# Kernel tuning notes

Hardware: AMD Instinct MI355X
Metric: run time of the kernel (lower is better)

The kernel has to match this reference:

```python
import jax, jax.numpy as jnp
import numpy as np
from jax import lax

NEG = -1e30  # effectively log(0), safe in float32 over long accumulations


def setup_inputs() -> dict:
    key = jax.random.key(0)
    k1, k2, k3, k4, k5 = jax.random.split(key, 5)
    T, B, L, S = 2048, 64, 64, 256
    inputs = jax.random.normal(k1, (T, B, L), dtype=jnp.float32)
    # module initializes transition to zeros; use small random values for a
    # non-degenerate reference (zeros make transition terms vanish)
    transition = 0.01 * jax.random.normal(k2, (L, L), dtype=jnp.float32)
    targets = jax.random.randint(k3, (B, S), 0, L)
    input_lengths = jax.random.randint(k4, (B,), T // 2, T + 1)
    target_lengths = jax.random.randint(k5, (B,), S // 4, S + 1)
    return {"inputs": inputs, "transition": transition, "targets": targets,
            "input_lengths": input_lengths, "target_lengths": target_lengths}


def _fcc(inputs, trans, input_lengths):
    # Fully-connected (partition) score: logsumexp over all label paths.
    # trans[i, j] = score of transitioning from label j to label i.
    T, B, L = inputs.shape
    def step(alpha, xt):
        x, t = xt
        # new[b,i] = x[b,i] + logsumexp_j(alpha[b,j] + trans[i,j])
        new = x + jax.scipy.special.logsumexp(alpha[:, None, :] + trans[None, :, :], axis=-1)
        alpha = jnp.where((t < input_lengths)[:, None], new, alpha)
        return alpha, None
    alpha, _ = lax.scan(step, inputs[0], (inputs[1:], jnp.arange(1, T)))
    return jax.scipy.special.logsumexp(alpha, axis=-1)  # [B]


def _fac(inputs, trans, targets, input_lengths, target_lengths):
    # Force-aligned score: logsumexp over monotonic alignments of targets.
    T, B, L = inputs.shape
    S = targets.shape[1]
    emit = inputs[:, jnp.arange(B)[:, None], targets]          # [T,B,S]
    self_tr = trans[targets, targets]                           # [B,S] stay score
    prev = jnp.concatenate([targets[:, :1], targets[:, :-1]], axis=1)
    move_tr = trans[targets, prev].at[:, 0].set(NEG)            # [B,S] advance score
    alpha0 = jnp.full((B, S), NEG, jnp.float32).at[:, 0].set(emit[0, :, 0])
    def step(alpha, et):
        e, t = et
        shifted = jnp.concatenate([jnp.full((B, 1), NEG, jnp.float32), alpha[:, :-1]], axis=1)
        new = e + jnp.logaddexp(alpha + self_tr, shifted + move_tr)
        alpha = jnp.where((t < input_lengths)[:, None], new, alpha)
        return alpha, None
    alpha, _ = lax.scan(step, alpha0, (emit[1:], jnp.arange(1, T)))
    return alpha[jnp.arange(B), target_lengths - 1]             # [B]


def reference(inputs, transition, targets, input_lengths, target_lengths):
    full = _fcc(inputs, transition, input_lengths)
    aligned = _fac(inputs, transition, targets, input_lengths, target_lengths)
    return jnp.mean(full - aligned)  # reduction='mean'
```

## Files before the change

kernel.cpp:

```cpp
#include <hip/hip_runtime.h>
#include <math.h>


constexpr int T_ = 2048, B_ = 64, L_ = 64, S_ = 256;
constexpr int CSEG = 64, NSEG = 32;
constexpr int FCH = 16;
constexpr float LN2 = 0.6931471805599453f;

typedef __bf16 bf16x8 __attribute__((ext_vector_type(8)));
typedef __bf16 bf16x4 __attribute__((ext_vector_type(4)));
typedef float f32x16 __attribute__((ext_vector_type(16)));

constexpr size_t OFF_SCALE = (size_t)NSEG * B_ * 4096 * 2;
constexpr size_t OFF_FULL = OFF_SCALE + (size_t)NSEG * B_ * 4;
constexpr size_t OFF_FWD = OFF_FULL + B_ * 4;
constexpr size_t OFF_BWD = OFF_FWD + (size_t)B_ * 256 * 8;
constexpr size_t OFF_LF = OFF_BWD + (size_t)B_ * 256 * 8;
constexpr size_t OFF_LB = OFF_LF + B_ * 4;

__device__ __forceinline__ float wave_max64(float v) {
#pragma unroll
  for (int off = 1; off < 64; off <<= 1) v = fmaxf(v, __shfl_xor(v, off, 64));
  return v;
}
__device__ __forceinline__ float wave_sum64(float v) {
#pragma unroll
  for (int off = 1; off < 64; off <<= 1) v += __shfl_xor(v, off, 64);
  return v;
}
__device__ __forceinline__ double wave_max64d(double v) {
#pragma unroll
  for (int off = 1; off < 64; off <<= 1) v = fmax(v, __shfl_xor(v, off, 64));
  return v;
}

struct P1shm {
  __align__(16) float xs[CSEG][64];
  __align__(16) float m_arr[CSEG];
  __align__(16) float redmax[4];
  __align__(16) __bf16 P[2][64 * 68];
};
struct FACshm {
  __align__(16) float E[2][FCH][64];
  __align__(16) float Eg[2][FCH][256];
  __align__(16) float m_fac[2][FCH];
  __align__(16) float mg[2][FCH];
};
union KU {
  P1shm p1;
  FACshm fac;
};

__global__ __launch_bounds__(256) void asg_k1(
    const float* __restrict__ inputs, const float* __restrict__ trans,
    const int* __restrict__ targets, const int* __restrict__ ilen,
    const int* __restrict__ tlenp, char* __restrict__ ws) {
  __shared__ KU u;
  const int tid = threadIdx.x, lane = tid & 63, wv = tid >> 6;
  const int bid = blockIdx.x;
  float* scales = (float*)(ws + OFF_SCALE);

  if (bid < 2 * B_) {
    const bool isfwd = (bid < B_);
    const int b = bid & 63;
    const int len = ilen[b];
    const int tl = tlenp[b];
    const int TS = (len - 1) >> 1;
    double* vecout = (double*)(ws + (isfwd ? OFF_FWD : OFF_BWD)) + b * 256;
    float* Lout = (float*)(ws + (isfwd ? OFF_LF : OFF_LB));

    int tg0 = 0, tg1 = 0, tg2 = 0, tg3 = 0;
    if (wv == 0 || wv == 2) {
      int4 t4 = *(const int4*)(targets + b * S_ + lane * 4);
      tg0 = t4.x; tg1 = t4.y; tg2 = t4.z; tg3 = t4.w;
    }
    auto stage = [&](int c, int buf) {
#pragma unroll
      for (int i = 0; i < 4; ++i) {
        int f = lane + 64 * i;
        int r = f >> 4, c4 = f & 15;
        int t = c * FCH + r;
        if (t > T_ - 1) t = T_ - 1;
        float4 v = *(const float4*)(inputs + (size_t)t * (B_ * L_) + b * L_ +
                                    c4 * 4);
        float m = fmaxf(fmaxf(v.x, v.y), fmaxf(v.z, v.w));
#pragma unroll
        for (int off = 1; off < 16; off <<= 1)
          m = fmaxf(m, __shfl_xor(m, off, 64));
        v.x = __expf(v.x - m); v.y = __expf(v.y - m);
        v.z = __expf(v.z - m); v.w = __expf(v.w - m);
        *(float4*)&u.fac.E[buf][r][c4 * 4] = v;
        if ((lane & 15) == 0) u.fac.m_fac[buf][r] = m;
      }
    };
    auto regather = [&](int c, int buf) {
#pragma unroll 4
      for (int r = 0; r < FCH; ++r) {
        float4 h;
        h.x = u.fac.E[buf][r][tg0]; h.y = u.fac.E[buf][r][tg1];
        h.z = u.fac.E[buf][r][tg2]; h.w = u.fac.E[buf][r][tg3];
        *(float4*)&u.fac.Eg[buf][r][lane * 4] = h;
      }
      if (lane < FCH) u.fac.mg[buf][lane] = u.fac.m_fac[buf][lane];
    };

    if (isfwd) {
      double sw0 = 0, sw1 = 0, sw2 = 0, sw3 = 0;
      double mw0 = 0, mw1 = 0, mw2 = 0, mw3 = 0;
      if (wv == 0) {
        int tgm1 = (lane > 0) ? targets[b * S_ + lane * 4 - 1] : 0;
        sw0 = exp((double)trans[tg0 * 64 + tg0]);
        sw1 = exp((double)trans[tg1 * 64 + tg1]);
        sw2 = exp((double)trans[tg2 * 64 + tg2]);
        sw3 = exp((double)trans[tg3 * 64 + tg3]);
        mw0 = (lane == 0) ? 0.0 : exp((double)trans[tg0 * 64 + tgm1]);
        mw1 = exp((double)trans[tg1 * 64 + tg0]);
        mw2 = exp((double)trans[tg2 * 64 + tg1]);
        mw3 = exp((double)trans[tg3 * 64 + tg2]);
      }
      if (wv == 1) { stage(0, 0); stage(1, 1); }
      __syncthreads();
      if (wv == 2) regather(0, 0);
      __syncthreads();

      double d0 = 0.0, d1 = 0.0, d2 = 0.0, d3 = 0.0, shv = 0.0;
      float Lacc = 0.0f;
      const int addr_up = ((lane + 63) & 63) << 2;
      if (wv == 0) {
        if (lane == 0) d0 = (double)u.fac.Eg[0][0][0];
        Lacc = u.fac.mg[0][0];
        __builtin_amdgcn_s_setprio(1);
      }
      for (int c = 0; 16 * c <= TS; ++c) {
        const int buf = c & 1;
        if (wv == 1) {
          if (16 * (c + 2) <= TS) stage(c + 2, buf);
        } else if (wv == 2) {
          if (16 * (c + 1) <= TS) regather(c + 1, buf ^ 1);
        } else if (wv == 0) {
          if (c) {
            double dmax = wave_max64d(fmax(fmax(d0, d1), fmax(d2, d3)));
            long long lm = __double_as_longlong(dmax);
            int ex = (int)((lm >> 52) & 0x7FF);
            double M = __longlong_as_double((long long)(2046 - ex) << 52);
            d0 *= M; d1 *= M; d2 *= M; d3 *= M; shv *= M;
            Lacc += (float)(ex - 1023) * LN2;
          }
          const int r0 = (c == 0) ? 1 : 0;
          const int rmax = min(FCH, TS + 1 - 16 * c);
          float4 eH = *(const float4*)&u.fac.Eg[buf][r0][lane * 4];
          float mH = u.fac.mg[buf][r0];
          const int r1 = min(r0 + 1, FCH - 1);
          float4 pH = *(const float4*)&u.fac.Eg[buf][r1][lane * 4];
          float pM = u.fac.mg[buf][r1];
          for (int r = r0; r < rmax; ++r) {
            const int rn = min(r + 2, FCH - 1);
            float4 nH = *(const float4*)&u.fac.Eg[buf][rn][lane * 4];
            float nM = u.fac.mg[buf][rn];
            double nd3 = (double)eH.w * fma(mw3, d2, sw3 * d3);
            long long l3 = __double_as_longlong(nd3);
            int slo = __builtin_amdgcn_ds_bpermute(addr_up, (int)l3);
            int shi = __builtin_amdgcn_ds_bpermute(addr_up, (int)(l3 >> 32));
            double nd0 = (double)eH.x * fma(mw0, shv, sw0 * d0);
            double nd1 = (double)eH.y * fma(mw1, d0, sw1 * d1);
            double nd2 = (double)eH.z * fma(mw2, d1, sw2 * d2);
            d0 = nd0; d1 = nd1; d2 = nd2; d3 = nd3;
            shv = __longlong_as_double(((long long)shi << 32) |
                                       (unsigned int)slo);
            Lacc += mH;
            eH = pH; mH = pM; pH = nH; pM = nM;
          }
        }
        __syncthreads();
      }
      if (wv == 0) {
        __builtin_amdgcn_s_setprio(0);
        vecout[lane * 4 + 0] = d0; vecout[lane * 4 + 1] = d1;
        vecout[lane * 4 + 2] = d2; vecout[lane * 4 + 3] = d3;
        if (lane == 0) Lout[b] = Lacc;
      }
    } else {
      double sw0 = 0, sw1 = 0, sw2 = 0, sw3 = 0;
      double mv0 = 0, mv1 = 0, mv2 = 0, mv3 = 0;
      if (wv == 0) {
        int tg4 = (lane < 63) ? targets[b * S_ + lane * 4 + 4] : 0;
        sw0 = exp((double)trans[tg0 * 64 + tg0]);
        sw1 = exp((double)trans[tg1 * 64 + tg1]);
        sw2 = exp((double)trans[tg2 * 64 + tg2]);
        sw3 = exp((double)trans[tg3 * 64 + tg3]);
        mv0 = exp((double)trans[tg1 * 64 + tg0]);
        mv1 = exp((double)trans[tg2 * 64 + tg1]);
        mv2 = exp((double)trans[tg3 * 64 + tg2]);
        mv3 = (lane < 63) ? exp((double)trans[tg4 * 64 + tg3]) : 0.0;
      }
      const int cmax = (len - 1) >> 4;
      const int cmin = (TS + 1) >> 4;
      if (wv == 1) {
        stage(cmax, cmax & 1);
        if (cmax - 1 >= cmin) stage(cmax - 1, (cmax - 1) & 1);
      }
      __syncthreads();
      if (wv == 2) regather(cmax, cmax & 1);
      __syncthreads();

      const int idx = tl - 1;
      double b0 = 0, b1 = 0, b2 = 0, b3 = 0, g0cur = 0, shg = 0;
      float Lacc = 0.0f;
      const int addr_dn = ((lane + 1) & 63) << 2;
      if (wv == 0) {
        b0 = (lane * 4 + 0 == idx) ? 1.0 : 0.0;
        b1 = (lane * 4 + 1 == idx) ? 1.0 : 0.0;
        b2 = (lane * 4 + 2 == idx) ? 1.0 : 0.0;
        b3 = (lane * 4 + 3 == idx) ? 1.0 : 0.0;
        const int rh0 = (len - 1) & 15;
        float e0x = u.fac.Eg[cmax & 1][rh0][lane * 4];
        g0cur = (double)e0x * b0;
        long long lg = __double_as_longlong(g0cur);
        int slo = __builtin_amdgcn_ds_bpermute(addr_dn, (int)lg);
        int shi = __builtin_amdgcn_ds_bpermute(addr_dn, (int)(lg >> 32));
        shg = __longlong_as_double(((long long)shi << 32) | (unsigned int)slo);
        __builtin_amdgcn_s_setprio(1);
      }
      for (int c = cmax; c >= cmin; --c) {
        const int buf = c & 1;
        if (wv == 1) {
          if (c - 2 >= cmin) stage(c - 2, buf);
        } else if (wv == 2) {
          if (c - 1 >= cmin) regather(c - 1, buf ^ 1);
        } else if (wv == 0) {
          if (c != cmax) {
            double dmax = wave_max64d(fmax(fmax(b0, b1), fmax(b2, b3)));
            long long lm = __double_as_longlong(dmax);
            int ex = (int)((lm >> 52) & 0x7FF);
            double M = __longlong_as_double((long long)(2046 - ex) << 52);
            b0 *= M; b1 *= M; b2 *= M; b3 *= M; g0cur *= M; shg *= M;
            Lacc += (float)(ex - 1023) * LN2;
          }
          const int rhi = (c == cmax) ? ((len - 1) & 15) : FCH - 1;
          const int rlo = max(0, (TS + 1) - 16 * c);
          float4 eH = *(const float4*)&u.fac.Eg[buf][rhi][lane * 4];
          float mH = u.fac.mg[buf][rhi];
          const int r1 = max(rhi - 1, rlo);
          float4 pH = *(const float4*)&u.fac.Eg[buf][r1][lane * 4];
          float pM = u.fac.mg[buf][r1];
          for (int r = rhi; r >= rlo; --r) {
            const int rn = max(r - 2, rlo);
            float4 nH = *(const float4*)&u.fac.Eg[buf][rn][lane * 4];
            float nM = u.fac.mg[buf][rn];
            double g1 = (double)eH.y * b1;
            double g2 = (double)eH.z * b2;
            double g3 = (double)eH.w * b3;
            double nb0 = fma(mv0, g1, sw0 * g0cur);
            double nb1 = fma(mv1, g2, sw1 * g1);
            double nb2 = fma(mv2, g3, sw2 * g2);
            double nb3 = fma(mv3, shg, sw3 * g3);
            double g0n = (double)pH.x * nb0;
            long long lg2 = __double_as_longlong(g0n);
            int slo2 = __builtin_amdgcn_ds_bpermute(addr_dn, (int)lg2);
            int shi2 = __builtin_amdgcn_ds_bpermute(addr_dn, (int)(lg2 >> 32));
            b0 = nb0; b1 = nb1; b2 = nb2; b3 = nb3;
            g0cur = g0n;
            shg = __longlong_as_double(((long long)shi2 << 32) |
                                       (unsigned int)slo2);
            Lacc += mH;
            eH = pH; mH = pM; pH = nH; pM = nM;
          }
        }
        __syncthreads();
      }
      if (wv == 0) {
        __builtin_amdgcn_s_setprio(0);
        vecout[lane * 4 + 0] = b0; vecout[lane * 4 + 1] = b1;
        vecout[lane * 4 + 2] = b2; vecout[lane * 4 + 3] = b3;
        if (lane == 0) Lout[b] = Lacc;
      }
    }
    return;
  }

  const int sid = bid - 2 * B_;
  const int b = sid >> 5, s = sid & 31;
  const int t0 = 1 + s * CSEG;
  const int len = ilen[b];
  int ke = min(CSEG, T_ - t0);
  ke = min(ke, len - t0);
  if (ke < 0) ke = 0;

#pragma unroll
  for (int i = 0; i < 4; ++i) {
    int f4 = tid + 256 * i;
    int r = f4 >> 4, c4 = f4 & 15;
    int t = t0 + r;
    if (t > T_ - 1) t = T_ - 1;
    float4 v = *(const float4*)(inputs + (size_t)t * (B_ * L_) + b * L_ + c4 * 4);
    *(float4*)(&u.p1.xs[r][c4 * 4]) = v;
  }
  __syncthreads();
#pragma unroll
  for (int rr = 0; rr < 16; ++rr) {
    int r = wv * 16 + rr;
    float v = wave_max64(u.p1.xs[r][lane]);
    if (lane == 0) u.p1.m_arr[r] = v;
  }
  __syncthreads();
#pragma unroll
  for (int i = 0; i < 4; ++i) {
    int f4 = tid + 256 * i;
    int r = f4 >> 4, c4 = f4 & 15;
    float m = u.p1.m_arr[r];
    float4 v = *(float4*)(&u.p1.xs[r][c4 * 4]);
    v.x = __expf(v.x - m); v.y = __expf(v.y - m);
    v.z = __expf(v.z - m); v.w = __expf(v.w - m);
    *(float4*)(&u.p1.xs[r][c4 * 4]) = v;
  }
  for (int i = tid; i < 64 * 68; i += 256) u.p1.P[0][i] = (__bf16)0.0f;
  __syncthreads();
  if (tid < 64) u.p1.P[0][tid * 68 + tid] = (__bf16)1.0f;

  const int ma = wv >> 1, nb = wv & 1;
  const int arow = 32 * ma + (lane & 31);
  const int hh = lane >> 5;
  const int coln = 32 * nb + (lane & 31);
  float Wf[4][8];
#pragma unroll
  for (int kc = 0; kc < 4; ++kc) {
    const float* tp = trans + arow * 64 + kc * 16 + hh * 8;
#pragma unroll
    for (int j = 0; j < 8; ++j) Wf[kc][j] = __expf(tp[j]);
  }

  float lsres = 0.0f;
  int cur = 0;
  for (int k = 0; k < ke; ++k) {
    __syncthreads();
    float scf = 1.0f;
    if ((k & 7) == 0 && k != 0) {
      float mm = fmaxf(fmaxf(u.p1.redmax[0], u.p1.redmax[1]),
                       fmaxf(u.p1.redmax[2], u.p1.redmax[3]));
      scf = __builtin_amdgcn_rcpf(mm);
      lsres += __logf(mm);
    }
    const float srow = u.p1.xs[k][arow] * scf;
    bf16x8 A[4], Bf[4];
    const __bf16* Pc = u.p1.P[cur];
#pragma unroll
    for (int kc = 0; kc < 4; ++kc) {
#pragma unroll
      for (int j = 0; j < 8; ++j) A[kc][j] = (__bf16)(Wf[kc][j] * srow);
      const __bf16* p = Pc + coln * 68 + kc * 16 + hh * 8;
      bf16x4 lo = *(const bf16x4*)p;
      bf16x4 hi = *(const bf16x4*)(p + 4);
      Bf[kc] = __builtin_shufflevector(lo, hi, 0, 1, 2, 3, 4, 5, 6, 7);
    }
    f32x16 acc;
#pragma unroll
    for (int e = 0; e < 16; ++e) acc[e] = 0.0f;
    acc = __builtin_amdgcn_mfma_f32_32x32x16_bf16(A[0], Bf[0], acc, 0, 0, 0);
    acc = __builtin_amdgcn_mfma_f32_32x32x16_bf16(A[1], Bf[1], acc, 0, 0, 0);
    acc = __builtin_amdgcn_mfma_f32_32x32x16_bf16(A[2], Bf[2], acc, 0, 0, 0);
    acc = __builtin_amdgcn_mfma_f32_32x32x16_bf16(A[3], Bf[3], acc, 0, 0, 0);
    __bf16* Pn = u.p1.P[cur ^ 1];
#pragma unroll
    for (int q = 0; q < 4; ++q) {
      const int i0 = 32 * ma + 8 * q + 4 * hh;
      bf16x4 w;
      w[0] = (__bf16)acc[4 * q + 0]; w[1] = (__bf16)acc[4 * q + 1];
      w[2] = (__bf16)acc[4 * q + 2]; w[3] = (__bf16)acc[4 * q + 3];
      *(bf16x4*)(Pn + coln * 68 + i0) = w;
    }
    if ((k & 7) == 7) {
      float mx = acc[0];
#pragma unroll
      for (int e = 1; e < 16; ++e) mx = fmaxf(mx, acc[e]);
      mx = wave_max64(mx);
      if (lane == 0) u.p1.redmax[wv] = mx;
    }
    cur ^= 1;
  }
  __syncthreads();
  __bf16* G = ((__bf16*)ws) + (size_t)sid * 4096;
  const __bf16* Pf = u.p1.P[cur];
  for (int i = tid; i < 4096; i += 256) G[i] = Pf[(i >> 6) * 68 + (i & 63)];
  if (wv == 0) {
    float mt = (lane < ke) ? u.p1.m_arr[lane] : 0.0f;
    float msum = wave_sum64(mt);
    if (lane == 0) scales[sid] = msum + lsres;
  }
}

__global__ __launch_bounds__(128) void asg_k2(const float* __restrict__ inputs,
                                              char* __restrict__ ws) {
  __shared__ __align__(16) float Gl[2][64][68];
  __shared__ __align__(16) float Eb[64];
  const int tid = threadIdx.x, lane = tid & 63, wv = tid >> 6;
  const int b = blockIdx.x;
  const __bf16* M = (const __bf16*)ws;
  const float* scales = (const float*)(ws + OFF_SCALE);
  float* full = (float*)(ws + OFF_FULL);

  auto stage = [&](int s, int buf) {
    const __bf16* g = M + ((size_t)(b * NSEG + s)) * 4096 + lane * 64;
#pragma unroll
    for (int q = 0; q < 8; ++q) {
      bf16x8 v = *(const bf16x8*)(g + q * 8);
      float4 f0{(float)v[0], (float)v[1], (float)v[2], (float)v[3]};
      float4 f1{(float)v[4], (float)v[5], (float)v[6], (float)v[7]};
      *(float4*)&Gl[buf][lane][q * 8] = f0;
      *(float4*)&Gl[buf][lane][q * 8 + 4] = f1;
    }
  };

  float Ev = 0.0f, ls = 0.0f;
  if (wv == 0) {
    float x0 = inputs[b * L_ + lane];
    float m0 = wave_max64(x0);
    Ev = __expf(x0 - m0);
    ls = m0;
    Eb[lane] = Ev;
  } else {
    stage(0, 0);
  }
  __syncthreads();
  for (int s = 0; s < NSEG; ++s) {
    if (wv == 1 && s + 1 < NSEG) stage(s + 1, (s + 1) & 1);
    if (wv == 0) {
      const int buf = s & 1;
      float ap0 = 0, ap1 = 0, ap2 = 0, ap3 = 0;
#pragma unroll
      for (int k4 = 0; k4 < 16; ++k4) {
        float4 e4 = *(const float4*)&Eb[k4 * 4];
        ap0 = fmaf(Gl[buf][4 * k4 + 0][lane], e4.x, ap0);
        ap1 = fmaf(Gl[buf][4 * k4 + 1][lane], e4.y, ap1);
        ap2 = fmaf(Gl[buf][4 * k4 + 2][lane], e4.z, ap2);
        ap3 = fmaf(Gl[buf][4 * k4 + 3][lane], e4.w, ap3);
      }
      float ap = (ap0 + ap1) + (ap2 + ap3);
      float mx = wave_max64(ap);
      float sc = __builtin_amdgcn_rcpf(mx);
      Ev = ap * sc;
      Eb[lane] = Ev;
      ls += __logf(mx) + scales[b * NSEG + s];
    }
    __syncthreads();
  }
  if (wv == 0) {
    float ssum = wave_sum64(Ev);
    if (lane == 0) full[b] = ls + __logf(ssum);
  }
}

__global__ __launch_bounds__(256) void asg_k3(const char* __restrict__ ws,
                                              float* __restrict__ out) {
  __shared__ float diff[64];
  const int tid = threadIdx.x;
  const int b = tid >> 2, q = tid & 3;
  const double* fv = (const double*)(ws + OFF_FWD) + b * 256;
  const double* bv = (const double*)(ws + OFF_BWD) + b * 256;
  const float* full = (const float*)(ws + OFF_FULL);
  const float* Lf = (const float*)(ws + OFF_LF);
  const float* Lb = (const float*)(ws + OFF_LB);

  double s = 0.0;
  for (int j = q * 64; j < q * 64 + 64; ++j) s += fv[j] * bv[j];
  s += __shfl_xor(s, 1, 64);
  s += __shfl_xor(s, 2, 64);
  if (q == 0) {
    s = fmax(s, 1e-300);
    long long ls = __double_as_longlong(s);
    int ex = (int)((ls >> 52) & 0x7FF);
    double mant = __longlong_as_double((ls & 0xFFFFFFFFFFFFFLL) |
                                       (1023LL << 52));
    float alig = Lf[b] + Lb[b] + (float)(ex - 1023) * LN2 + __logf((float)mant);
    diff[b] = full[b] - alig;
  }
  __syncthreads();
  if (tid < 64) {
    float d = diff[tid];
    d = wave_sum64(d);
    if (tid == 0) out[0] = d * (1.0f / 64.0f);
  }
}

extern "C" void kernel_launch(void* const* d_in, const int* in_sizes, int n_in,
                              void* d_out, int out_size, void* d_ws,
                              size_t ws_size, hipStream_t stream) {
  const float* inputs = (const float*)d_in[0];
  const float* trans = (const float*)d_in[1];
  const int* targets = (const int*)d_in[2];
  const int* ilen = (const int*)d_in[3];
  const int* tlen = (const int*)d_in[4];
  char* ws = (char*)d_ws;
  float* out = (float*)d_out;

  hipLaunchKernelGGL(asg_k1, dim3(2 * B_ + NSEG * B_), dim3(256), 0, stream,
                     inputs, trans, targets, ilen, tlen, ws);
  hipLaunchKernelGGL(asg_k2, dim3(B_), dim3(128), 0, stream, inputs, ws);
  hipLaunchKernelGGL(asg_k3, dim3(1), dim3(256), 0, stream, ws, out);
}
```

Before: 197.5 us.

## Run each segment matrix-product chain in a single wave without block barriers

Each FCC segment's 64x64 transfer-matrix product chain now runs in one wavefront that computes all four 32x32 MFMA tiles, so the per-step __syncthreads is gone. Two segments share a block, which halves the segment grid; waves 2-3 of those blocks exit early. The emission scaling moves from the A operand (W*x) to a post-MFMA row scale with precomputed bf16 exp(trans). Emissions are stored as bf16 and max reductions use shuffles. The trade-off is less parallelism per segment and longer serial work per wave, in exchange for no barrier latency.

```diff
diff --git a/kernel.cpp b/kernel.cpp
--- a/kernel.cpp
+++ b/kernel.cpp
@@ -34,11 +34,13 @@
   return v;
 }
 
+struct P1W {
+  __align__(16) __bf16 P[2][64 * 68];
+  __align__(16) __bf16 xs[64][72];
+  __align__(16) float m[64];
+};
 struct P1shm {
-  __align__(16) float xs[CSEG][64];
-  __align__(16) float m_arr[CSEG];
-  __align__(16) float redmax[4];
-  __align__(16) __bf16 P[2][64 * 68];
+  P1W w[2];
 };
 struct FACshm {
   __align__(16) float E[2][FCH][64];
@@ -278,114 +280,120 @@
     return;
   }
 
-  const int sid = bid - 2 * B_;
+  if (wv >= 2) return;
+  const int sid = (bid - 2 * B_) * 2 + wv;
   const int b = sid >> 5, s = sid & 31;
   const int t0 = 1 + s * CSEG;
   const int len = ilen[b];
+  P1W& W = u.p1.w[wv];
+  const int hh = lane >> 5;
   int ke = min(CSEG, T_ - t0);
   ke = min(ke, len - t0);
   if (ke < 0) ke = 0;
 
 #pragma unroll
-  for (int i = 0; i < 4; ++i) {
-    int f4 = tid + 256 * i;
-    int r = f4 >> 4, c4 = f4 & 15;
+  for (int i = 0; i < 16; ++i) {
+    int f = lane + 64 * i;
+    int r = f >> 4, c4 = f & 15;
     int t = t0 + r;
     if (t > T_ - 1) t = T_ - 1;
     float4 v = *(const float4*)(inputs + (size_t)t * (B_ * L_) + b * L_ + c4 * 4);
-    *(float4*)(&u.p1.xs[r][c4 * 4]) = v;
-  }
-  __syncthreads();
-#pragma unroll
-  for (int rr = 0; rr < 16; ++rr) {
-    int r = wv * 16 + rr;
-    float v = wave_max64(u.p1.xs[r][lane]);
-    if (lane == 0) u.p1.m_arr[r] = v;
-  }
-  __syncthreads();
-#pragma unroll
-  for (int i = 0; i < 4; ++i) {
-    int f4 = tid + 256 * i;
-    int r = f4 >> 4, c4 = f4 & 15;
-    float m = u.p1.m_arr[r];
-    float4 v = *(float4*)(&u.p1.xs[r][c4 * 4]);
-    v.x = __expf(v.x - m); v.y = __expf(v.y - m);
-    v.z = __expf(v.z - m); v.w = __expf(v.w - m);
-    *(float4*)(&u.p1.xs[r][c4 * 4]) = v;
-  }
-  for (int i = tid; i < 64 * 68; i += 256) u.p1.P[0][i] = (__bf16)0.0f;
-  __syncthreads();
-  if (tid < 64) u.p1.P[0][tid * 68 + tid] = (__bf16)1.0f;
-
-  const int ma = wv >> 1, nb = wv & 1;
-  const int arow = 32 * ma + (lane & 31);
-  const int hh = lane >> 5;
-  const int coln = 32 * nb + (lane & 31);
-  float Wf[4][8];
-#pragma unroll
-  for (int kc = 0; kc < 4; ++kc) {
-    const float* tp = trans + arow * 64 + kc * 16 + hh * 8;
-#pragma unroll
-    for (int j = 0; j < 8; ++j) Wf[kc][j] = __expf(tp[j]);
-  }
-
-  float lsres = 0.0f;
+    float m = fmaxf(fmaxf(v.x, v.y), fmaxf(v.z, v.w));
+#pragma unroll
+    for (int off = 1; off < 16; off <<= 1)
+      m = fmaxf(m, __shfl_xor(m, off, 64));
+    bf16x4 h;
+    h[0] = (__bf16)__expf(v.x - m); h[1] = (__bf16)__expf(v.y - m);
+    h[2] = (__bf16)__expf(v.z - m); h[3] = (__bf16)__expf(v.w - m);
+    *(bf16x4*)&W.xs[r][c4 * 4] = h;
+    if ((lane & 15) == 0) W.m[r] = m;
+  }
+  for (int i = lane; i < 64 * 68; i += 64) W.P[0][i] = (__bf16)0.0f;
+  W.P[0][lane * 68 + lane] = (__bf16)1.0f;
+
+  bf16x8 Wb[2][4];
+#pragma unroll
+  for (int ma = 0; ma < 2; ++ma) {
+#pragma unroll
+    for (int kc = 0; kc < 4; ++kc) {
+      const float* tp = trans + (32 * ma + (lane & 31)) * 64 + kc * 16 + hh * 8;
+      float4 ta = *(const float4*)tp;
+      float4 tb = *(const float4*)(tp + 4);
+      bf16x8 w;
+      w[0] = (__bf16)__expf(ta.x); w[1] = (__bf16)__expf(ta.y);
+      w[2] = (__bf16)__expf(ta.z); w[3] = (__bf16)__expf(ta.w);
+      w[4] = (__bf16)__expf(tb.x); w[5] = (__bf16)__expf(tb.y);
+      w[6] = (__bf16)__expf(tb.z); w[7] = (__bf16)__expf(tb.w);
+      Wb[ma][kc] = w;
+    }
+  }
+
+  const int c0 = lane & 31;
+  float lsres = 0.0f, redmax_r = 1.0f;
   int cur = 0;
   for (int k = 0; k < ke; ++k) {
-    __syncthreads();
     float scf = 1.0f;
     if ((k & 7) == 0 && k != 0) {
-      float mm = fmaxf(fmaxf(u.p1.redmax[0], u.p1.redmax[1]),
-                       fmaxf(u.p1.redmax[2], u.p1.redmax[3]));
-      scf = __builtin_amdgcn_rcpf(mm);
-      lsres += __logf(mm);
-    }
-    const float srow = u.p1.xs[k][arow] * scf;
-    bf16x8 A[4], Bf[4];
-    const __bf16* Pc = u.p1.P[cur];
+      scf = __builtin_amdgcn_rcpf(redmax_r);
+      lsres += __logf(redmax_r);
+    }
+    const __bf16* Pc = W.P[cur];
+    f32x16 a00, a01, a10, a11;
+#pragma unroll
+    for (int e = 0; e < 16; ++e) { a00[e] = 0; a01[e] = 0; a10[e] = 0; a11[e] = 0; }
 #pragma unroll
     for (int kc = 0; kc < 4; ++kc) {
-#pragma unroll
-      for (int j = 0; j < 8; ++j) A[kc][j] = (__bf16)(Wf[kc][j] * srow);
-      const __bf16* p = Pc + coln * 68 + kc * 16 + hh * 8;
-      bf16x4 lo = *(const bf16x4*)p;
-      bf16x4 hi = *(const bf16x4*)(p + 4);
-      Bf[kc] = __builtin_shufflevector(lo, hi, 0, 1, 2, 3, 4, 5, 6, 7);
-    }
-    f32x16 acc;
-#pragma unroll
-    for (int e = 0; e < 16; ++e) acc[e] = 0.0f;
-    acc = __builtin_amdgcn_mfma_f32_32x32x16_bf16(A[0], Bf[0], acc, 0, 0, 0);
-    acc = __builtin_amdgcn_mfma_f32_32x32x16_bf16(A[1], Bf[1], acc, 0, 0, 0);
-    acc = __builtin_amdgcn_mfma_f32_32x32x16_bf16(A[2], Bf[2], acc, 0, 0, 0);
-    acc = __builtin_amdgcn_mfma_f32_32x32x16_bf16(A[3], Bf[3], acc, 0, 0, 0);
-    __bf16* Pn = u.p1.P[cur ^ 1];
+      bf16x8 B0 = *(const bf16x8*)(Pc + c0 * 68 + kc * 16 + hh * 8);
+      bf16x8 B1 = *(const bf16x8*)(Pc + (32 + c0) * 68 + kc * 16 + hh * 8);
+      a00 = __builtin_amdgcn_mfma_f32_32x32x16_bf16(Wb[0][kc], B0, a00, 0, 0, 0);
+      a01 = __builtin_amdgcn_mfma_f32_32x32x16_bf16(Wb[0][kc], B1, a01, 0, 0, 0);
+      a10 = __builtin_amdgcn_mfma_f32_32x32x16_bf16(Wb[1][kc], B0, a10, 0, 0, 0);
+      a11 = __builtin_amdgcn_mfma_f32_32x32x16_bf16(Wb[1][kc], B1, a11, 0, 0, 0);
+    }
+    __bf16* Pn = W.P[cur ^ 1];
+    const bool track = ((k & 7) == 7);
+    float mx = 0.0f;
 #pragma unroll
     for (int q = 0; q < 4; ++q) {
-      const int i0 = 32 * ma + 8 * q + 4 * hh;
-      bf16x4 w;
-      w[0] = (__bf16)acc[4 * q + 0]; w[1] = (__bf16)acc[4 * q + 1];
-      w[2] = (__bf16)acc[4 * q + 2]; w[3] = (__bf16)acc[4 * q + 3];
-      *(bf16x4*)(Pn + coln * 68 + i0) = w;
-    }
-    if ((k & 7) == 7) {
-      float mx = acc[0];
-#pragma unroll
-      for (int e = 1; e < 16; ++e) mx = fmaxf(mx, acc[e]);
-      mx = wave_max64(mx);
-      if (lane == 0) u.p1.redmax[wv] = mx;
-    }
+      const int i0 = 8 * q + 4 * hh;
+      bf16x4 ev = *(const bf16x4*)&W.xs[k][i0];
+      bf16x4 w0, w1;
+#pragma unroll
+      for (int j = 0; j < 4; ++j) {
+        float ef = (float)ev[j] * scf;
+        float s0 = a00[4 * q + j] * ef;
+        float s1 = a01[4 * q + j] * ef;
+        if (track) mx = fmaxf(mx, fmaxf(s0, s1));
+        w0[j] = (__bf16)s0; w1[j] = (__bf16)s1;
+      }
+      *(bf16x4*)(Pn + c0 * 68 + i0) = w0;
+      *(bf16x4*)(Pn + (32 + c0) * 68 + i0) = w1;
+    }
+#pragma unroll
+    for (int q = 0; q < 4; ++q) {
+      const int i0 = 32 + 8 * q + 4 * hh;
+      bf16x4 ev = *(const bf16x4*)&W.xs[k][i0];
+      bf16x4 w0, w1;
+#pragma unroll
+      for (int j = 0; j < 4; ++j) {
+        float ef = (float)ev[j] * scf;
+        float s0 = a10[4 * q + j] * ef;
+        float s1 = a11[4 * q + j] * ef;
+        if (track) mx = fmaxf(mx, fmaxf(s0, s1));
+        w0[j] = (__bf16)s0; w1[j] = (__bf16)s1;
+      }
+      *(bf16x4*)(Pn + c0 * 68 + i0) = w0;
+      *(bf16x4*)(Pn + (32 + c0) * 68 + i0) = w1;
+    }
+    if (track) redmax_r = wave_max64(mx);
     cur ^= 1;
   }
-  __syncthreads();
   __bf16* G = ((__bf16*)ws) + (size_t)sid * 4096;
-  const __bf16* Pf = u.p1.P[cur];
-  for (int i = tid; i < 4096; i += 256) G[i] = Pf[(i >> 6) * 68 + (i & 63)];
-  if (wv == 0) {
-    float mt = (lane < ke) ? u.p1.m_arr[lane] : 0.0f;
-    float msum = wave_sum64(mt);
-    if (lane == 0) scales[sid] = msum + lsres;
-  }
+  const __bf16* Pf = W.P[cur];
+  for (int i = lane; i < 4096; i += 64) G[i] = Pf[(i >> 6) * 68 + (i & 63)];
+  float mt = (lane < ke) ? W.m[lane] : 0.0f;
+  float msum = wave_sum64(mt);
+  if (lane == 0) scales[sid] = msum + lsres;
 }
 
 __global__ __launch_bounds__(128) void asg_k2(const float* __restrict__ inputs,
@@ -492,8 +500,8 @@
   char* ws = (char*)d_ws;
   float* out = (float*)d_out;
 
-  hipLaunchKernelGGL(asg_k1, dim3(2 * B_ + NSEG * B_), dim3(256), 0, stream,
-                     inputs, trans, targets, ilen, tlen, ws);
+  hipLaunchKernelGGL(asg_k1, dim3(2 * B_ + NSEG * B_ / 2), dim3(256), 0,
+                     stream, inputs, trans, targets, ilen, tlen, ws);
   hipLaunchKernelGGL(asg_k2, dim3(B_), dim3(128), 0, stream, inputs, ws);
   hipLaunchKernelGGL(asg_k3, dim3(1), dim3(256), 0, stream, ws, out);
 }
```

Measured after the change: 393.4 us. 1.99x slower.

## Store staged exponentials in half precision and fuse row-max into load

Applied to the files above, without the earlier changes.

Shared-memory staging buffers for the force-aligned and partition passes now hold fp16/bf16 exponentials instead of fp32, with padded rows. In the partition segment kernel, the row-max reduction and exp are fused into the global load using 16-lane shuffles, which removes two block barriers and a shared-memory round trip. The recursion wave's scheduling priority is raised from 1 to 2. Together these aim to cut LDS traffic and barrier count, at the cost of reduced precision in the emission terms.

```diff
diff --git a/kernel.cpp b/kernel.cpp
--- a/kernel.cpp
+++ b/kernel.cpp
@@ -10,6 +10,7 @@
 typedef __bf16 bf16x8 __attribute__((ext_vector_type(8)));
 typedef __bf16 bf16x4 __attribute__((ext_vector_type(4)));
 typedef float f32x16 __attribute__((ext_vector_type(16)));
+typedef _Float16 f16x4 __attribute__((ext_vector_type(4)));
 
 constexpr size_t OFF_SCALE = (size_t)NSEG * B_ * 4096 * 2;
 constexpr size_t OFF_FULL = OFF_SCALE + (size_t)NSEG * B_ * 4;
@@ -35,14 +36,14 @@
 }
 
 struct P1shm {
-  __align__(16) float xs[CSEG][64];
+  __align__(16) __bf16 xs[CSEG][68];
   __align__(16) float m_arr[CSEG];
   __align__(16) float redmax[4];
   __align__(16) __bf16 P[2][64 * 68];
 };
 struct FACshm {
-  __align__(16) float E[2][FCH][64];
-  __align__(16) float Eg[2][FCH][256];
+  __align__(16) _Float16 E[2][FCH][68];
+  __align__(16) _Float16 Eg[2][FCH][256];
   __align__(16) float m_fac[2][FCH];
   __align__(16) float mg[2][FCH];
 };
@@ -87,19 +88,20 @@
 #pragma unroll
         for (int off = 1; off < 16; off <<= 1)
           m = fmaxf(m, __shfl_xor(m, off, 64));
-        v.x = __expf(v.x - m); v.y = __expf(v.y - m);
-        v.z = __expf(v.z - m); v.w = __expf(v.w - m);
-        *(float4*)&u.fac.E[buf][r][c4 * 4] = v;
+        f16x4 h;
+        h[0] = (_Float16)__expf(v.x - m); h[1] = (_Float16)__expf(v.y - m);
+        h[2] = (_Float16)__expf(v.z - m); h[3] = (_Float16)__expf(v.w - m);
+        *(f16x4*)&u.fac.E[buf][r][c4 * 4] = h;
         if ((lane & 15) == 0) u.fac.m_fac[buf][r] = m;
       }
     };
     auto regather = [&](int c, int buf) {
 #pragma unroll 4
       for (int r = 0; r < FCH; ++r) {
-        float4 h;
-        h.x = u.fac.E[buf][r][tg0]; h.y = u.fac.E[buf][r][tg1];
-        h.z = u.fac.E[buf][r][tg2]; h.w = u.fac.E[buf][r][tg3];
-        *(float4*)&u.fac.Eg[buf][r][lane * 4] = h;
+        f16x4 h;
+        h[0] = u.fac.E[buf][r][tg0]; h[1] = u.fac.E[buf][r][tg1];
+        h[2] = u.fac.E[buf][r][tg2]; h[3] = u.fac.E[buf][r][tg3];
+        *(f16x4*)&u.fac.Eg[buf][r][lane * 4] = h;
       }
       if (lane < FCH) u.fac.mg[buf][lane] = u.fac.m_fac[buf][lane];
     };
@@ -127,9 +129,9 @@
       float Lacc = 0.0f;
       const int addr_up = ((lane + 63) & 63) << 2;
       if (wv == 0) {
-        if (lane == 0) d0 = (double)u.fac.Eg[0][0][0];
+        if (lane == 0) d0 = (double)(float)u.fac.Eg[0][0][0];
         Lacc = u.fac.mg[0][0];
-        __builtin_amdgcn_s_setprio(1);
+        __builtin_amdgcn_s_setprio(2);
       }
       for (int c = 0; 16 * c <= TS; ++c) {
         const int buf = c & 1;
@@ -148,22 +150,22 @@
           }
           const int r0 = (c == 0) ? 1 : 0;
           const int rmax = min(FCH, TS + 1 - 16 * c);
-          float4 eH = *(const float4*)&u.fac.Eg[buf][r0][lane * 4];
+          f16x4 eH = *(const f16x4*)&u.fac.Eg[buf][r0][lane * 4];
           float mH = u.fac.mg[buf][r0];
           const int r1 = min(r0 + 1, FCH - 1);
-          float4 pH = *(const float4*)&u.fac.Eg[buf][r1][lane * 4];
+          f16x4 pH = *(const f16x4*)&u.fac.Eg[buf][r1][lane * 4];
           float pM = u.fac.mg[buf][r1];
           for (int r = r0; r < rmax; ++r) {
             const int rn = min(r + 2, FCH - 1);
-            float4 nH = *(const float4*)&u.fac.Eg[buf][rn][lane * 4];
+            f16x4 nH = *(const f16x4*)&u.fac.Eg[buf][rn][lane * 4];
             float nM = u.fac.mg[buf][rn];
-            double nd3 = (double)eH.w * fma(mw3, d2, sw3 * d3);
+            double nd3 = (double)(float)eH[3] * fma(mw3, d2, sw3 * d3);
             long long l3 = __double_as_longlong(nd3);
             int slo = __builtin_amdgcn_ds_bpermute(addr_up, (int)l3);
             int shi = __builtin_amdgcn_ds_bpermute(addr_up, (int)(l3 >> 32));
-            double nd0 = (double)eH.x * fma(mw0, shv, sw0 * d0);
-            double nd1 = (double)eH.y * fma(mw1, d0, sw1 * d1);
-            double nd2 = (double)eH.z * fma(mw2, d1, sw2 * d2);
+            double nd0 = (double)(float)eH[0] * fma(mw0, shv, sw0 * d0);
+            double nd1 = (double)(float)eH[1] * fma(mw1, d0, sw1 * d1);
+            double nd2 = (double)(float)eH[2] * fma(mw2, d1, sw2 * d2);
             d0 = nd0; d1 = nd1; d2 = nd2; d3 = nd3;
             shv = __longlong_as_double(((long long)shi << 32) |
                                        (unsigned int)slo);
@@ -213,13 +215,13 @@
         b2 = (lane * 4 + 2 == idx) ? 1.0 : 0.0;
         b3 = (lane * 4 + 3 == idx) ? 1.0 : 0.0;
         const int rh0 = (len - 1) & 15;
-        float e0x = u.fac.Eg[cmax & 1][rh0][lane * 4];
+        float e0x = (float)u.fac.Eg[cmax & 1][rh0][lane * 4];
         g0cur = (double)e0x * b0;
         long long lg = __double_as_longlong(g0cur);
         int slo = __builtin_amdgcn_ds_bpermute(addr_dn, (int)lg);
         int shi = __builtin_amdgcn_ds_bpermute(addr_dn, (int)(lg >> 32));
         shg = __longlong_as_double(((long long)shi << 32) | (unsigned int)slo);
-        __builtin_amdgcn_s_setprio(1);
+        __builtin_amdgcn_s_setprio(2);
       }
       for (int c = cmax; c >= cmin; --c) {
         const int buf = c & 1;
@@ -238,23 +240,23 @@
           }
           const int rhi = (c == cmax) ? ((len - 1) & 15) : FCH - 1;
           const int rlo = max(0, (TS + 1) - 16 * c);
-          float4 eH = *(const float4*)&u.fac.Eg[buf][rhi][lane * 4];
+          f16x4 eH = *(const f16x4*)&u.fac.Eg[buf][rhi][lane * 4];
           float mH = u.fac.mg[buf][rhi];
           const int r1 = max(rhi - 1, rlo);
-          float4 pH = *(const float4*)&u.fac.Eg[buf][r1][lane * 4];
+          f16x4 pH = *(const f16x4*)&u.fac.Eg[buf][r1][lane * 4];
           float pM = u.fac.mg[buf][r1];
           for (int r = rhi; r >= rlo; --r) {
             const int rn = max(r - 2, rlo);
-            float4 nH = *(const float4*)&u.fac.Eg[buf][rn][lane * 4];
+            f16x4 nH = *(const f16x4*)&u.fac.Eg[buf][rn][lane * 4];
             float nM = u.fac.mg[buf][rn];
-            double g1 = (double)eH.y * b1;
-            double g2 = (double)eH.z * b2;
-            double g3 = (double)eH.w * b3;
+            double g1 = (double)(float)eH[1] * b1;
+            double g2 = (double)(float)eH[2] * b2;
+            double g3 = (double)(float)eH[3] * b3;
             double nb0 = fma(mv0, g1, sw0 * g0cur);
             double nb1 = fma(mv1, g2, sw1 * g1);
             double nb2 = fma(mv2, g3, sw2 * g2);
             double nb3 = fma(mv3, shg, sw3 * g3);
-            double g0n = (double)pH.x * nb0;
+            double g0n = (double)(float)pH[0] * nb0;
             long long lg2 = __double_as_longlong(g0n);
             int slo2 = __builtin_amdgcn_ds_bpermute(addr_dn, (int)lg2);
             int shi2 = __builtin_amdgcn_ds_bpermute(addr_dn, (int)(lg2 >> 32));
@@ -293,25 +295,15 @@
     int t = t0 + r;
     if (t > T_ - 1) t = T_ - 1;
     float4 v = *(const float4*)(inputs + (size_t)t * (B_ * L_) + b * L_ + c4 * 4);
-    *(float4*)(&u.p1.xs[r][c4 * 4]) = v;
-  }
-  __syncthreads();
-#pragma unroll
-  for (int rr = 0; rr < 16; ++rr) {
-    int r = wv * 16 + rr;
-    float v = wave_max64(u.p1.xs[r][lane]);
-    if (lane == 0) u.p1.m_arr[r] = v;
-  }
-  __syncthreads();
-#pragma unroll
-  for (int i = 0; i < 4; ++i) {
-    int f4 = tid + 256 * i;
-    int r = f4 >> 4, c4 = f4 & 15;
-    float m = u.p1.m_arr[r];
-    float4 v = *(float4*)(&u.p1.xs[r][c4 * 4]);
-    v.x = __expf(v.x - m); v.y = __expf(v.y - m);
-    v.z = __expf(v.z - m); v.w = __expf(v.w - m);
-    *(float4*)(&u.p1.xs[r][c4 * 4]) = v;
+    float m = fmaxf(fmaxf(v.x, v.y), fmaxf(v.z, v.w));
+#pragma unroll
+    for (int off = 1; off < 16; off <<= 1)
+      m = fmaxf(m, __shfl_xor(m, off, 64));
+    bf16x4 h;
+    h[0] = (__bf16)__expf(v.x - m); h[1] = (__bf16)__expf(v.y - m);
+    h[2] = (__bf16)__expf(v.z - m); h[3] = (__bf16)__expf(v.w - m);
+    *(bf16x4*)&u.p1.xs[r][c4 * 4] = h;
+    if ((lane & 15) == 0) u.p1.m_arr[r] = m;
   }
   for (int i = tid; i < 64 * 68; i += 256) u.p1.P[0][i] = (__bf16)0.0f;
   __syncthreads();
@@ -340,7 +332,7 @@
       scf = __builtin_amdgcn_rcpf(mm);
       lsres += __logf(mm);
     }
-    const float srow = u.p1.xs[k][arow] * scf;
+    const float srow = (float)u.p1.xs[k][arow] * scf;
     bf16x8 A[4], Bf[4];
     const __bf16* Pc = u.p1.P[cur];
 #pragma unroll
```

After: 195.1 us (median of 2 runs). Within noise of the previous version (-1.2%).
